# Kernel optimization log

Measured on AMD Instinct MI355X. Metric: run time of the kernel, lower is better.

## Reference

```python
import jax, jax.numpy as jnp
import numpy as np

N_NODES = 20000
N_EDGES = 320000
N_GRAPHS = 64


def gat_conv(x, src, dst, W, a_src, a_dst, bias, heads, ch, concat):
    # x: [N, F_in]; W: [F_in, heads*ch]; a_src/a_dst: [heads, ch]
    N = x.shape[0]
    h = (x @ W).reshape(N, heads, ch)                       # [N, H, C]
    alpha_s = jnp.sum(h * a_src, axis=-1)                   # [N, H]
    alpha_d = jnp.sum(h * a_dst, axis=-1)                   # [N, H]
    e = jax.nn.leaky_relu(alpha_s[src] + alpha_d[dst], 0.2) # [E, H]
    # segment softmax over incoming edges of each destination node
    m = jax.ops.segment_max(e, dst, num_segments=N)         # [N, H]
    ex = jnp.exp(e - m[dst])
    denom = jax.ops.segment_sum(ex, dst, num_segments=N)    # [N, H]
    alpha = ex / (denom[dst] + 1e-16)                       # [E, H]
    msg = h[src] * alpha[:, :, None]                        # [E, H, C]
    out = jax.ops.segment_sum(msg, dst, num_segments=N)     # [N, H, C]
    out = out.reshape(N, heads * ch) if concat else out.mean(axis=1)
    return out + bias, alpha


def setup_inputs() -> dict:
    key = jax.random.key(0)
    ks = jax.random.split(key, 24)
    dim_in, md, dim_out = 8, 64, 128
    hid = md * 4  # 256
    p = lambda k, shape: jax.random.normal(k, shape, dtype=jnp.float32) * 0.1
    inp = {
        "x_ppi": jax.random.normal(ks[0], (N_NODES, dim_in), dtype=jnp.float32),
        "ppi_edge_index": jax.random.randint(ks[1], (2, N_EDGES), 0, N_NODES),
        "ppi_batch": jnp.sort(jax.random.randint(ks[2], (N_NODES,), 0, N_GRAPHS)),
        # GATConv 1: dim_in -> 64, heads=4, concat
        "W1": p(ks[3], (dim_in, 4 * md)), "a_src1": p(ks[4], (4, md)), "a_dst1": p(ks[5], (4, md)), "b_gat1": jnp.zeros((hid,), jnp.float32),
        "lw1": p(ks[6], (dim_in, hid)), "lb1": jnp.zeros((hid,), jnp.float32),
        # GATConv 2: 256 -> 64, heads=4, concat
        "W2": p(ks[7], (hid, 4 * md)), "a_src2": p(ks[8], (4, md)), "a_dst2": p(ks[9], (4, md)), "b_gat2": jnp.zeros((hid,), jnp.float32),
        "lw2": p(ks[10], (hid, hid)), "lb2": jnp.zeros((hid,), jnp.float32),
        # GATConv 3: 256 -> 128, heads=6, concat=False (mean)
        "W3": p(ks[11], (hid, 6 * dim_out)), "a_src3": p(ks[12], (6, dim_out)), "a_dst3": p(ks[13], (6, dim_out)), "b_gat3": jnp.zeros((dim_out,), jnp.float32),
        "lw3": p(ks[14], (hid, dim_out)), "lb3": jnp.zeros((dim_out,), jnp.float32),
        # BatchNorm1d(dim_out), training-mode batch statistics
        "bn_gamma": jnp.ones((dim_out,), jnp.float32), "bn_beta": jnp.zeros((dim_out,), jnp.float32),
    }
    return inp


def reference(x_ppi, ppi_edge_index, ppi_batch,
              W1, a_src1, a_dst1, b_gat1, lw1, lb1,
              W2, a_src2, a_dst2, b_gat2, lw2, lb2,
              W3, a_src3, a_dst3, b_gat3, lw3, lb3,
              bn_gamma, bn_beta):
    src, dst = ppi_edge_index[0], ppi_edge_index[1]
    g1, _ = gat_conv(x_ppi, src, dst, W1, a_src1, a_dst1, b_gat1, heads=4, ch=64, concat=True)
    x = jax.nn.relu(g1 + x_ppi @ lw1 + lb1)
    g2, _ = gat_conv(x, src, dst, W2, a_src2, a_dst2, b_gat2, heads=4, ch=64, concat=True)
    x = jax.nn.relu(g2 + x @ lw2 + lb2)
    x_res = x @ lw3 + lb3
    g3, att = gat_conv(x, src, dst, W3, a_src3, a_dst3, b_gat3, heads=6, ch=128, concat=False)
    x = g3 + x_res
    x = jax.nn.relu(x)
    # BatchNorm1d, training mode (biased variance, eps=1e-5)
    mu = x.mean(axis=0)
    var = jnp.mean((x - mu) ** 2, axis=0)
    x = (x - mu) * jax.lax.rsqrt(var + 1e-5) * bn_gamma + bn_beta
    # global max pool over graphs
    pooled = jax.ops.segment_max(x, ppi_batch, num_segments=N_GRAPHS)
    return pooled, att
```

## Files before the change

### kernel.cpp

```cpp
#include <hip/hip_runtime.h>
#include <hip/hip_bf16.h>
#include <math.h>

#define N_NODES 20000
#define N_EDGES 320000
#define N_GRAPHS 64

typedef __bf16 bf16_t;
typedef bf16_t bf16x8 __attribute__((ext_vector_type(8)));
typedef bf16_t bf16x4 __attribute__((ext_vector_type(4)));
typedef bf16_t bf16x2 __attribute__((ext_vector_type(2)));
typedef float f32x4 __attribute__((ext_vector_type(4)));
typedef float f32x2 __attribute__((ext_vector_type(2)));

__global__ void hist_k(const int* __restrict__ dst, int* __restrict__ deg, int E) {
    int e = blockIdx.x * 256 + threadIdx.x;
    if (e < E) atomicAdd(&deg[dst[e]], 1);
}

__global__ __launch_bounds__(1024) void scan_k(const int* __restrict__ deg,
                                               int* __restrict__ offs,
                                               int* __restrict__ cursor, int n) {
    __shared__ int s_ws[16];
    int tid = threadIdx.x;
    int lane = tid & 63, w = tid >> 6;
    int carry = 0;
    for (int base = 0; base < n; base += 1024) {
        int i = base + tid;
        int v = (i < n) ? deg[i] : 0;
        int x = v;
        #pragma unroll
        for (int off = 1; off < 64; off <<= 1) {
            int t = __shfl_up(x, off);
            if (lane >= off) x += t;
        }
        if (lane == 63) s_ws[w] = x;
        __syncthreads();
        if (tid < 16) {
            int y = s_ws[tid];
            #pragma unroll
            for (int off = 1; off < 16; off <<= 1) {
                int t = __shfl_up(y, off);
                if (tid >= off) y += t;
            }
            s_ws[tid] = y;
        }
        __syncthreads();
        int wbase = (w > 0) ? s_ws[w - 1] : 0;
        int ex = carry + wbase + x - v;
        if (i < n) { offs[i] = ex; cursor[i] = ex; }
        carry += s_ws[15];
        __syncthreads();
    }
    if (tid == 0) offs[n] = carry;
}

__global__ void scatter_k(const int* __restrict__ src, const int* __restrict__ dst,
                          int* __restrict__ cursor, int* __restrict__ csr_src,
                          int* __restrict__ csr_eid, int E) {
    int e = blockIdx.x * 256 + threadIdx.x;
    if (e < E) {
        int d = dst[e];
        int p = atomicAdd(&cursor[d], 1);
        csr_src[p] = src[e];
        csr_eid[p] = e;
    }
}

__global__ __launch_bounds__(256) void wt_k(const float* __restrict__ W,
                                            bf16_t* __restrict__ Bt, int K, int N) {
    __shared__ float t[32][33];
    int k0 = blockIdx.y * 32, n0 = blockIdx.x * 32;
    int tx = threadIdx.x & 31, ty = threadIdx.x >> 5;
    for (int i = ty; i < 32; i += 8) t[i][tx] = W[(size_t)(k0 + i) * N + n0 + tx];
    __syncthreads();
    for (int i = ty; i < 32; i += 8)
        Bt[(size_t)(n0 + i) * K + k0 + tx] = (bf16_t)t[tx][i];
}

__global__ void w3s_k(const float* __restrict__ W3, const float* __restrict__ lw3,
                      bf16_t* __restrict__ Bt) {
    int id = blockIdx.x * 256 + threadIdx.x;
    if (id >= 128 * 1792) return;
    int n = id / 1792, k = id - n * 1792;
    float v;
    if (k < 1536) {
        int h = k >> 8, c = k & 255;
        v = W3[(size_t)c * 768 + h * 128 + n] * (1.f / 6.f);
    } else {
        int c = k - 1536;
        v = lw3[(size_t)c * 128 + n];
    }
    Bt[id] = (bf16_t)v;
}

__global__ void b40_k(const float* __restrict__ W1, const float* __restrict__ lw1,
                      float* __restrict__ B) {
    int id = blockIdx.x * 256 + threadIdx.x;
    if (id >= 40 * 256) return;
    int k = id >> 8, n = id & 255;
    float v;
    if (k < 32) {
        int h = k >> 3, c = k & 7;
        v = ((n >> 6) == h) ? W1[(size_t)c * 256 + n] : 0.f;
    } else {
        int c = k - 32;
        v = lw1[(size_t)c * 256 + n];
    }
    B[id] = v;
}

__global__ void va_k(const float* __restrict__ W, const float* __restrict__ a_s,
                     const float* __restrict__ a_d, float* __restrict__ Va,
                     float* __restrict__ Vd, int H, int C) {
    int k = blockIdx.x;
    int lane = threadIdx.x;
    const float* wr = W + (size_t)k * H * C;
    for (int h = 0; h < H; ++h) {
        float sa = 0.f, sd = 0.f;
        for (int c = lane; c < C; c += 64) {
            float wv = wr[h * C + c];
            sa += wv * a_s[h * C + c];
            sd += wv * a_d[h * C + c];
        }
        #pragma unroll
        for (int m = 32; m; m >>= 1) { sa += __shfl_xor(sa, m); sd += __shfl_xor(sd, m); }
        if (lane == 0) { Va[k * H + h] = sa; Vd[k * H + h] = sd; }
    }
}

__global__ void addb_k(const float* __restrict__ a, const float* __restrict__ b,
                       float* __restrict__ o, int n) {
    int i = blockIdx.x * 256 + threadIdx.x;
    if (i < n) o[i] = a[i] + b[i];
}

template <typename OUT>
__global__ __launch_bounds__(256) void gemm_k(const float* __restrict__ A,
                                              const float* __restrict__ B,
                                              OUT* __restrict__ C,
                                              const float* __restrict__ bias,
                                              int M, int N, int K, int relu) {
    __shared__ float As[16][65];
    __shared__ float Bs[16][64];
    int tid = threadIdx.x;
    int tx = tid & 15, ty = tid >> 4;
    int row0 = blockIdx.y * 64, col0 = blockIdx.x * 64;
    float acc[4][4] = {};
    for (int k0 = 0; k0 < K; k0 += 16) {
        #pragma unroll
        for (int i = 0; i < 4; ++i) {
            int idx = tid + i * 256;
            int m = idx >> 4, kk = idx & 15;
            int gm = row0 + m, gk = k0 + kk;
            As[kk][m] = (gm < M && gk < K) ? A[(size_t)gm * K + gk] : 0.f;
        }
        #pragma unroll
        for (int i = 0; i < 4; ++i) {
            int idx = tid + i * 256;
            int kk = idx >> 6, n = idx & 63;
            int gk = k0 + kk, gn = col0 + n;
            Bs[kk][n] = (gk < K && gn < N) ? B[(size_t)gk * N + gn] : 0.f;
        }
        __syncthreads();
        #pragma unroll
        for (int kk = 0; kk < 16; ++kk) {
            float a[4], b[4];
            #pragma unroll
            for (int i = 0; i < 4; ++i) a[i] = As[kk][ty * 4 + i];
            #pragma unroll
            for (int j = 0; j < 4; ++j) b[j] = Bs[kk][tx * 4 + j];
            #pragma unroll
            for (int i = 0; i < 4; ++i)
                #pragma unroll
                for (int j = 0; j < 4; ++j) acc[i][j] += a[i] * b[j];
        }
        __syncthreads();
    }
    #pragma unroll
    for (int i = 0; i < 4; ++i) {
        int gm = row0 + ty * 4 + i;
        if (gm >= M) continue;
        #pragma unroll
        for (int j = 0; j < 4; ++j) {
            int gn = col0 + tx * 4 + j;
            if (gn < N) {
                float r = acc[i][j] + (bias ? bias[gn] : 0.f);
                if (relu) r = fmaxf(r, 0.f);
                C[(size_t)gm * N + gn] = (OUT)r;
            }
        }
    }
}

template <typename OUT>
__global__ __launch_bounds__(256) void gemm_bf16_k(
    const bf16_t* __restrict__ A, const bf16_t* __restrict__ Bt,
    OUT* __restrict__ C, const float* __restrict__ bias, int M, int N, int K,
    const float* __restrict__ asv, const float* __restrict__ adv,
    float* __restrict__ as_o, float* __restrict__ ad_o, int H, int Ch, int relu) {
    __shared__ bf16_t As[128][40];
    __shared__ bf16_t Bs[128][40];
    int tid = threadIdx.x;
    int row0 = blockIdx.y * 128, col0 = blockIdx.x * 128;
    int wave = tid >> 6, lane = tid & 63, quad = lane >> 4, l16 = lane & 15;
    int wm = wave >> 1, wn = wave & 1;
    f32x4 acc[4][4] = {};
    int sr = tid >> 2;
    int sc = (tid & 3) * 8;
    for (int k0 = 0; k0 < K; k0 += 32) {
        #pragma unroll
        for (int half = 0; half < 2; ++half) {
            int r = sr + half * 64;
            int gm = row0 + r;
            bf16x8 v = {};
            if (gm < M) v = *(const bf16x8*)&A[(size_t)gm * K + k0 + sc];
            *(bf16x8*)&As[r][sc] = v;
            int gn = col0 + r;
            bf16x8 w = {};
            if (gn < N) w = *(const bf16x8*)&Bt[(size_t)gn * K + k0 + sc];
            *(bf16x8*)&Bs[r][sc] = w;
        }
        __syncthreads();
        bf16x8 af[4], bfr[4];
        #pragma unroll
        for (int i = 0; i < 4; ++i) {
            af[i] = *(const bf16x8*)&As[wm * 64 + i * 16 + l16][quad * 8];
            bfr[i] = *(const bf16x8*)&Bs[wn * 64 + i * 16 + l16][quad * 8];
        }
        #pragma unroll
        for (int i = 0; i < 4; ++i)
            #pragma unroll
            for (int j = 0; j < 4; ++j)
                acc[i][j] = __builtin_amdgcn_mfma_f32_16x16x32_bf16(af[i], bfr[j],
                                                                   acc[i][j], 0, 0, 0);
        __syncthreads();
    }
    #pragma unroll
    for (int i = 0; i < 4; ++i) {
        int base_m = row0 + wm * 64 + i * 16 + quad * 4;
        #pragma unroll
        for (int j = 0; j < 4; ++j) {
            int gn = col0 + wn * 64 + j * 16 + l16;
            float bv = bias ? bias[gn] : 0.f;
            #pragma unroll
            for (int r = 0; r < 4; ++r) {
                int gm = base_m + r;
                if (gm < M) {
                    float rr = acc[i][j][r] + bv;
                    if (relu) rr = fmaxf(rr, 0.f);
                    C[(size_t)gm * N + gn] = (OUT)rr;
                }
            }
        }
    }
    if (asv) {
        int hd = (col0 + wn * 64) / Ch;
        float av[4], dv[4];
        #pragma unroll
        for (int j = 0; j < 4; ++j) {
            int ca = col0 + wn * 64 + j * 16 + l16;
            av[j] = asv[ca];
            dv[j] = adv[ca];
        }
        #pragma unroll
        for (int i = 0; i < 4; ++i) {
            float sp[4] = {}, sd[4] = {};
            #pragma unroll
            for (int j = 0; j < 4; ++j)
                #pragma unroll
                for (int r = 0; r < 4; ++r) {
                    sp[r] += acc[i][j][r] * av[j];
                    sd[r] += acc[i][j][r] * dv[j];
                }
            #pragma unroll
            for (int m = 1; m < 16; m <<= 1)
                #pragma unroll
                for (int r = 0; r < 4; ++r) {
                    sp[r] += __shfl_xor(sp[r], m);
                    sd[r] += __shfl_xor(sd[r], m);
                }
            if (l16 == 0) {
                #pragma unroll
                for (int r = 0; r < 4; ++r) {
                    int gm = row0 + wm * 64 + i * 16 + quad * 4 + r;
                    if (gm < M) {
                        as_o[gm * H + hd] = sp[r];
                        ad_o[gm * H + hd] = sd[r];
                    }
                }
            }
        }
    }
}

__global__ __launch_bounds__(256) void gemm_bf16_thin_k(
    const bf16_t* __restrict__ A, const bf16_t* __restrict__ Bt,
    float* __restrict__ C, const float* __restrict__ bias, int M, int N, int K) {
    __shared__ bf16_t As[32][40];
    __shared__ bf16_t Bs[64][40];
    int tid = threadIdx.x;
    int row0 = blockIdx.y * 32, col0 = blockIdx.x * 64;
    int wave = tid >> 6, lane = tid & 63, quad = lane >> 4, l16 = lane & 15;
    int wr = wave & 1;
    int wc = wave >> 1;
    f32x4 acc[2] = {};
    int ar = tid >> 2, ac = (tid & 3) * 8;
    for (int k0 = 0; k0 < K; k0 += 32) {
        if (tid < 128) {
            int gm = row0 + ar;
            bf16x8 v = {};
            if (gm < M) v = *(const bf16x8*)&A[(size_t)gm * K + k0 + ac];
            *(bf16x8*)&As[ar][ac] = v;
        }
        *(bf16x8*)&Bs[ar][ac] = *(const bf16x8*)&Bt[(size_t)(col0 + ar) * K + k0 + ac];
        __syncthreads();
        bf16x8 af = *(const bf16x8*)&As[wr * 16 + l16][quad * 8];
        #pragma unroll
        for (int j = 0; j < 2; ++j) {
            bf16x8 bf = *(const bf16x8*)&Bs[wc * 32 + j * 16 + l16][quad * 8];
            acc[j] = __builtin_amdgcn_mfma_f32_16x16x32_bf16(af, bf, acc[j], 0, 0, 0);
        }
        __syncthreads();
    }
    #pragma unroll
    for (int j = 0; j < 2; ++j) {
        int gn = col0 + wc * 32 + j * 16 + l16;
        float bv = bias[gn];
        #pragma unroll
        for (int r = 0; r < 4; ++r) {
            int gm = row0 + wr * 16 + quad * 4 + r;
            if (gm < M) C[(size_t)gm * N + gn] = fmaxf(acc[j][r] + bv, 0.f);
        }
    }
}

__device__ __forceinline__ float leaky02(float v) { return v > 0.f ? v : 0.2f * v; }

__global__ void asad1_k(const float* __restrict__ x, const float* __restrict__ Va,
                        const float* __restrict__ Vd, float* __restrict__ as_,
                        float* __restrict__ ad_, int N) {
    int idx = blockIdx.x * 256 + threadIdx.x;
    if (idx >= N * 4) return;
    int j = idx >> 2, h = idx & 3;
    const float* xr = x + (size_t)j * 8;
    float sa = 0.f, sd = 0.f;
    #pragma unroll
    for (int c = 0; c < 8; ++c) {
        sa += xr[c] * Va[c * 4 + h];
        sd += xr[c] * Vd[c * 4 + h];
    }
    as_[idx] = sa;
    ad_[idx] = sd;
}

__global__ void asad3_k(const bf16_t* __restrict__ xb, const float* __restrict__ Va,
                        const float* __restrict__ Vd, float* __restrict__ as_,
                        float* __restrict__ ad_) {
    int j = blockIdx.x;
    int lane = threadIdx.x;
    bf16x4 v = *(const bf16x4*)&xb[(size_t)j * 256 + lane * 4];
    float sa[6] = {}, sd[6] = {};
    #pragma unroll
    for (int i = 0; i < 4; ++i) {
        int k = lane * 4 + i;
        float xv = (float)v[i];
        #pragma unroll
        for (int h = 0; h < 6; ++h) {
            sa[h] += xv * Va[k * 6 + h];
            sd[h] += xv * Vd[k * 6 + h];
        }
    }
    #pragma unroll
    for (int h = 0; h < 6; ++h) {
        float a = sa[h], d = sd[h];
        #pragma unroll
        for (int m = 32; m; m >>= 1) { a += __shfl_xor(a, m); d += __shfl_xor(d, m); }
        if (lane == 0) { as_[j * 6 + h] = a; ad_[j * 6 + h] = d; }
    }
}

__global__ __launch_bounds__(256) void agg_z1_k(
    const float* __restrict__ x, const float* __restrict__ as_,
    const float* __restrict__ ad_, const int* __restrict__ offs,
    const int* __restrict__ csr_src, float* __restrict__ z1) {
    int j = blockIdx.x * 4 + (threadIdx.x >> 6);
    int t = threadIdx.x & 63;
    int e_l = t >> 3, c = t & 7;
    int o0 = offs[j], deg = offs[j + 1] - o0;
    float adj0 = ad_[j * 4 + 0], adj1 = ad_[j * 4 + 1];
    float adj2 = ad_[j * 4 + 2], adj3 = ad_[j * 4 + 3];
    float acc[4] = {}, ws[4] = {};
    for (int e0 = 0; e0 < deg; e0 += 8) {
        int ne = min(8, deg - e0);
        if (e_l < ne) {
            int s = csr_src[o0 + e0 + e_l];
            float xv = x[(size_t)s * 8 + c];
            f32x4 a = *(const f32x4*)&as_[s * 4];
            float w0 = __expf(leaky02(a[0] + adj0));
            float w1 = __expf(leaky02(a[1] + adj1));
            float w2 = __expf(leaky02(a[2] + adj2));
            float w3 = __expf(leaky02(a[3] + adj3));
            acc[0] += w0 * xv; acc[1] += w1 * xv;
            acc[2] += w2 * xv; acc[3] += w3 * xv;
            ws[0] += w0; ws[1] += w1; ws[2] += w2; ws[3] += w3;
        }
    }
    #pragma unroll
    for (int m = 8; m < 64; m <<= 1)
        #pragma unroll
        for (int h = 0; h < 4; ++h) {
            acc[h] += __shfl_xor(acc[h], m);
            ws[h] += __shfl_xor(ws[h], m);
        }
    if (e_l == 0) {
        #pragma unroll
        for (int h = 0; h < 4; ++h)
            z1[(size_t)j * 40 + h * 8 + c] = acc[h] / (ws[h] + 1e-16f);
        z1[(size_t)j * 40 + 32 + c] = x[(size_t)j * 8 + c];
    }
}

__global__ __launch_bounds__(256) void agg_concat_k(
    const bf16_t* __restrict__ h, const float* __restrict__ as_,
    const float* __restrict__ ad_, const int* __restrict__ offs,
    const int* __restrict__ csr_src, const float* __restrict__ lin,
    const float* __restrict__ bgat, bf16_t* __restrict__ xb) {
    int j = blockIdx.x;
    int tid = threadIdx.x;
    int o0 = offs[j], deg = offs[j + 1] - o0;
    __shared__ int s_src[64];
    __shared__ float s_adj[4];
    __shared__ float s_ws[8][4];
    __shared__ float s_inv[4];
    __shared__ float s_red[8][256];
    if (tid < 4) s_adj[tid] = ad_[j * 4 + tid];
    int g = tid >> 5;
    int u = tid & 31;
    int myh = u >> 3;
    const char* hbase = (const char*)h + u * 16;
    f32x4 acc0 = {}, acc1 = {};
    float wsum = 0.f;
    for (int e0 = 0; e0 < deg; e0 += 64) {
        int ne = min(64, deg - e0);
        if (tid < ne) s_src[tid] = csr_src[o0 + e0 + tid];
        __syncthreads();
        float adj = s_adj[myh];
        #pragma unroll 2
        for (int e = g; e < ne; e += 8) {
            int s = s_src[e];
            float w = __expf(leaky02(as_[s * 4 + myh] + adj));
            bf16x8 v = *(const bf16x8*)(hbase + (size_t)s * 512);
            wsum += w;
            #pragma unroll
            for (int i = 0; i < 4; ++i) acc0[i] += w * (float)v[i];
            #pragma unroll
            for (int i = 0; i < 4; ++i) acc1[i] += w * (float)v[4 + i];
        }
        __syncthreads();
    }
    if ((u & 7) == 0) s_ws[g][myh] = wsum;
    *(f32x4*)&s_red[g][u * 8] = acc0;
    *(f32x4*)&s_red[g][u * 8 + 4] = acc1;
    __syncthreads();
    if (tid < 4) {
        float d = 0.f;
        #pragma unroll
        for (int g2 = 0; g2 < 8; ++g2) d += s_ws[g2][tid];
        s_inv[tid] = 1.f / (d + 1e-16f);
    }
    __syncthreads();
    {
        int c = tid;
        float s = 0.f;
        #pragma unroll
        for (int g2 = 0; g2 < 8; ++g2) s += s_red[g2][c];
        float v = fmaxf(s * s_inv[c >> 6] + bgat[c] + lin[(size_t)j * 256 + c], 0.f);
        xb[(size_t)j * 256 + c] = (bf16_t)v;
    }
}

__global__ __launch_bounds__(192) void agg_z3_k(
    const bf16_t* __restrict__ xb, const float* __restrict__ as_,
    const float* __restrict__ ad_, const int* __restrict__ offs,
    const int* __restrict__ csr_src, const int* __restrict__ csr_eid,
    bf16_t* __restrict__ z, float* __restrict__ att) {
    int j = blockIdx.x;
    int tid = threadIdx.x;
    int o0 = offs[j], deg = offs[j + 1] - o0;
    __shared__ float s_adj[6];
    __shared__ int s_src[64];
    __shared__ float s_w[64 * 6];
    __shared__ float s_inv[6];
    if (tid < 6) s_adj[tid] = ad_[j * 6 + tid];
    __syncthreads();
    int h = tid >> 5;
    int c = tid & 31;
    const char* xbase = (const char*)xb + c * 16;
    f32x4 a0 = {}, a1 = {};
    float wsum = 0.f;
    for (int e0 = 0; e0 < deg; e0 += 64) {
        int ne = min(64, deg - e0);
        #pragma unroll
        for (int base = 0; base < 2; ++base) {
            int idx = tid + base * 192;
            if (idx < ne * 6) {
                int e = idx / 6, hh = idx - e * 6;
                int s = csr_src[o0 + e0 + e];
                if (hh == 0) s_src[e] = s;
                s_w[idx] = __expf(leaky02(as_[s * 6 + hh] + s_adj[hh]));
            }
        }
        __syncthreads();
        #pragma unroll 4
        for (int e = 0; e < ne; ++e) {
            int s = s_src[e];
            float w = s_w[e * 6 + h];
            bf16x8 v = *(const bf16x8*)(xbase + (size_t)s * 512);
            wsum += w;
            #pragma unroll
            for (int i = 0; i < 4; ++i) a0[i] += w * (float)v[i];
            #pragma unroll
            for (int i = 0; i < 4; ++i) a1[i] += w * (float)v[4 + i];
        }
        __syncthreads();
    }
    float inv = 1.f / (wsum + 1e-16f);
    {
        bf16x8 o;
        #pragma unroll
        for (int i = 0; i < 4; ++i) o[i] = (bf16_t)(a0[i] * inv);
        #pragma unroll
        for (int i = 0; i < 4; ++i) o[4 + i] = (bf16_t)(a1[i] * inv);
        *(bf16x8*)&z[(size_t)j * 1792 + h * 256 + c * 8] = o;
    }
    if (tid < 32)
        *(bf16x8*)&z[(size_t)j * 1792 + 1536 + tid * 8] =
            *(const bf16x8*)&xb[(size_t)j * 256 + tid * 8];
    if (c == 0) s_inv[h] = inv;
    __syncthreads();
    for (int idx = tid; idx < deg * 6; idx += 192) {
        int e = idx / 6, hh = idx - e * 6;
        int p = o0 + e;
        int s = csr_src[p];
        att[(size_t)csr_eid[p] * 6 + hh] =
            __expf(leaky02(as_[s * 6 + hh] + s_adj[hh])) * s_inv[hh];
    }
}

__global__ void bn_stats_k(const float* __restrict__ y, float* __restrict__ sums, int N) {
    int c = threadIdx.x;
    float s = 0.f, q = 0.f;
    for (int r = blockIdx.x; r < N; r += gridDim.x) {
        float v = y[(size_t)r * 128 + c];
        s += v;
        q += v * v;
    }
    atomicAdd(&sums[c], s);
    atomicAdd(&sums[128 + c], q);
}
__global__ void bn_scale_k(const float* __restrict__ sums, const float* __restrict__ gamma,
                           const float* __restrict__ beta, float* __restrict__ scale,
                           float* __restrict__ shift, int N) {
    int c = threadIdx.x;
    float mu = sums[c] / (float)N;
    float var = fmaxf(sums[128 + c] / (float)N - mu * mu, 0.f);
    float inv = rsqrtf(var + 1e-5f) * gamma[c];
    scale[c] = inv;
    shift[c] = beta[c] - mu * inv;
}

__device__ __forceinline__ unsigned f2key(float f) {
    unsigned b = __float_as_uint(f);
    return (b & 0x80000000u) ? ~b : (b | 0x80000000u);
}
__global__ void pool_init_k(unsigned* __restrict__ pool_u) {
    int i = blockIdx.x * 256 + threadIdx.x;
    if (i < N_GRAPHS * 128) pool_u[i] = f2key(-3.402823466e38f * 2.0f);
}
__global__ void norm_pool_k(const float* __restrict__ y, const float* __restrict__ scale,
                            const float* __restrict__ shift, const int* __restrict__ batch,
                            unsigned* __restrict__ pool_u, int N) {
    int idx = blockIdx.x * 256 + threadIdx.x;
    if (idx >= N * 128) return;
    int n = idx >> 7, c = idx & 127;
    float v = y[idx] * scale[c] + shift[c];
    atomicMax(&pool_u[batch[n] * 128 + c], f2key(v));
}
__global__ void pool_write_k(const unsigned* __restrict__ pool_u, float* __restrict__ out) {
    int i = blockIdx.x * 256 + threadIdx.x;
    if (i < N_GRAPHS * 128) {
        unsigned u = pool_u[i];
        unsigned b = (u & 0x80000000u) ? (u & 0x7FFFFFFFu) : ~u;
        out[i] = __uint_as_float(b);
    }
}

extern "C" void kernel_launch(void* const* d_in, const int* in_sizes, int n_in,
                              void* d_out, int out_size, void* d_ws, size_t ws_size,
                              hipStream_t stream) {
    const int N = N_NODES, E = N_EDGES;
    const float* x_ppi = (const float*)d_in[0];
    const int* edge = (const int*)d_in[1];
    const int* batch = (const int*)d_in[2];
    const float* W1 = (const float*)d_in[3];
    const float* a_src1 = (const float*)d_in[4];
    const float* a_dst1 = (const float*)d_in[5];
    const float* b_gat1 = (const float*)d_in[6];
    const float* lw1 = (const float*)d_in[7];
    const float* lb1 = (const float*)d_in[8];
    const float* W2 = (const float*)d_in[9];
    const float* a_src2 = (const float*)d_in[10];
    const float* a_dst2 = (const float*)d_in[11];
    const float* b_gat2 = (const float*)d_in[12];
    const float* lw2 = (const float*)d_in[13];
    const float* lb2 = (const float*)d_in[14];
    const float* W3 = (const float*)d_in[15];
    const float* a_src3 = (const float*)d_in[16];
    const float* a_dst3 = (const float*)d_in[17];
    const float* b_gat3 = (const float*)d_in[18];
    const float* lw3 = (const float*)d_in[19];
    const float* lb3 = (const float*)d_in[20];
    const float* bn_gamma = (const float*)d_in[21];
    const float* bn_beta = (const float*)d_in[22];

    const int* src = edge;
    const int* dst = edge + E;

    size_t off = 0;
    auto alloc = [&](size_t bytes) {
        size_t o = off;
        off = (off + bytes + 255) & ~(size_t)255;
        return o;
    };
    char* ws = (char*)d_ws;
    bf16_t* xb = (bf16_t*)(ws + alloc((size_t)N * 256 * 2));
    bf16_t* zbig = (bf16_t*)(ws + alloc((size_t)N * 1792 * 2));
    bf16_t* hb = zbig;
    bf16_t* z3 = zbig;
    float* lin = (float*)(ws + alloc((size_t)N * 256 * 4));
    float* z1 = (float*)(ws + alloc((size_t)N * 40 * 4));
    float* as_ = (float*)(ws + alloc((size_t)N * 6 * 4));
    float* ad_ = (float*)(ws + alloc((size_t)N * 6 * 4));
    int* deg = (int*)(ws + alloc((size_t)(N + 1) * 4));
    int* offs = (int*)(ws + alloc((size_t)(N + 1) * 4));
    int* cursor = (int*)(ws + alloc((size_t)(N + 1) * 4));
    int* csr_src = (int*)(ws + alloc((size_t)E * 4));
    int* csr_eid = (int*)(ws + alloc((size_t)E * 4));
    bf16_t* Wt2 = (bf16_t*)(ws + alloc((size_t)256 * 256 * 2));
    bf16_t* lwt2 = (bf16_t*)(ws + alloc((size_t)256 * 256 * 2));
    bf16_t* Bt3s = (bf16_t*)(ws + alloc((size_t)128 * 1792 * 2));
    float* B40 = (float*)(ws + alloc((size_t)40 * 256 * 4));
    float* Va1 = (float*)(ws + alloc(8 * 4 * 4));
    float* Vd1 = (float*)(ws + alloc(8 * 4 * 4));
    float* Va3 = (float*)(ws + alloc(256 * 6 * 4));
    float* Vd3 = (float*)(ws + alloc(256 * 6 * 4));
    float* bias1s = (float*)(ws + alloc(256 * 4));
    float* bias3s = (float*)(ws + alloc(128 * 4));
    float* bn_sums = (float*)(ws + alloc(256 * 4));
    float* bn_scale = (float*)(ws + alloc(128 * 4));
    float* bn_shift = (float*)(ws + alloc(128 * 4));
    unsigned* pool_u = (unsigned*)(ws + alloc((size_t)N_GRAPHS * 128 * 4));

    float* out_pool = (float*)d_out;
    float* out_att = (float*)d_out + N_GRAPHS * 128;

    hipMemsetAsync(deg, 0, (size_t)N * 4, stream);
    hist_k<<<(E + 255) / 256, 256, 0, stream>>>(dst, deg, E);
    scan_k<<<1, 1024, 0, stream>>>(deg, offs, cursor, N);
    scatter_k<<<(E + 255) / 256, 256, 0, stream>>>(src, dst, cursor, csr_src, csr_eid, E);
    wt_k<<<dim3(8, 8), 256, 0, stream>>>(W2, Wt2, 256, 256);
    wt_k<<<dim3(8, 8), 256, 0, stream>>>(lw2, lwt2, 256, 256);
    w3s_k<<<896, 256, 0, stream>>>(W3, lw3, Bt3s);
    b40_k<<<40, 256, 0, stream>>>(W1, lw1, B40);
    va_k<<<8, 64, 0, stream>>>(W1, a_src1, a_dst1, Va1, Vd1, 4, 64);
    va_k<<<256, 64, 0, stream>>>(W3, a_src3, a_dst3, Va3, Vd3, 6, 128);
    addb_k<<<1, 256, 0, stream>>>(lb1, b_gat1, bias1s, 256);
    addb_k<<<1, 128, 0, stream>>>(lb3, b_gat3, bias3s, 128);

    asad1_k<<<(N * 4 + 255) / 256, 256, 0, stream>>>(x_ppi, Va1, Vd1, as_, ad_, N);
    agg_z1_k<<<N / 4, 256, 0, stream>>>(x_ppi, as_, ad_, offs, csr_src, z1);
    gemm_k<bf16_t><<<dim3(4, 313), 256, 0, stream>>>(z1, B40, xb, bias1s, N, 256, 40, 1);

    gemm_bf16_k<bf16_t><<<dim3(2, 157), 256, 0, stream>>>(xb, Wt2, hb, nullptr, N, 256, 256,
                                                          a_src2, a_dst2, as_, ad_, 4, 64, 0);
    gemm_bf16_k<float><<<dim3(2, 157), 256, 0, stream>>>(xb, lwt2, lin, lb2, N, 256, 256,
                                                         nullptr, nullptr, nullptr, nullptr,
                                                         0, 1, 0);
    agg_concat_k<<<N, 256, 0, stream>>>(hb, as_, ad_, offs, csr_src, lin, b_gat2, xb);

    float* y = lin;
    asad3_k<<<N, 64, 0, stream>>>(xb, Va3, Vd3, as_, ad_);
    agg_z3_k<<<N, 192, 0, stream>>>(xb, as_, ad_, offs, csr_src, csr_eid, z3, out_att);
    gemm_bf16_thin_k<<<dim3(2, 625), 256, 0, stream>>>(z3, Bt3s, y, bias3s, N, 128, 1792);

    hipMemsetAsync(bn_sums, 0, 256 * 4, stream);
    bn_stats_k<<<160, 128, 0, stream>>>(y, bn_sums, N);
    bn_scale_k<<<1, 128, 0, stream>>>(bn_sums, bn_gamma, bn_beta, bn_scale, bn_shift, N);

    pool_init_k<<<(N_GRAPHS * 128 + 255) / 256, 256, 0, stream>>>(pool_u);
    norm_pool_k<<<((size_t)N * 128 + 255) / 256, 256, 0, stream>>>(y, bn_scale, bn_shift, batch,
                                                                   pool_u, N);
    pool_write_k<<<(N_GRAPHS * 128 + 255) / 256, 256, 0, stream>>>(pool_u, out_pool);
}
```

Before: 466.1 us.

## Compute layer-3 per-head weighted aggregation with MFMA over edge tiles

Rewrites agg_z3_k so that, for each chunk of 32 incoming edges, it stages the bf16 attention weights (6 heads padded to 16) and the gathered neighbour features (transposed) in shared memory. It then computes the weighted sums for all heads at once with 16x16x32 bf16 MFMA, replacing the scalar per-head FMA loop. Neighbour rows are now gathered once per chunk and shared by all heads instead of being reloaded by every head group. The trade-offs are rounding the weights to bf16, wasted MFMA rows from the head padding, a transpose through LDS with possible bank conflicts, and a block size raised from 192 to 256.

Result: slower. 503.1 us (+7.9%).

```diff
diff --git a/kernel.cpp b/kernel.cpp
--- a/kernel.cpp
+++ b/kernel.cpp
@@ -480,7 +480,7 @@
     }
 }
 
-__global__ __launch_bounds__(192) void agg_z3_k(
+__global__ __launch_bounds__(256) void agg_z3_k(
     const bf16_t* __restrict__ xb, const float* __restrict__ as_,
     const float* __restrict__ ad_, const int* __restrict__ offs,
     const int* __restrict__ csr_src, const int* __restrict__ csr_eid,
@@ -489,57 +489,79 @@
     int tid = threadIdx.x;
     int o0 = offs[j], deg = offs[j + 1] - o0;
     __shared__ float s_adj[6];
-    __shared__ int s_src[64];
-    __shared__ float s_w[64 * 6];
+    __shared__ int s_src[32];
+    __shared__ bf16_t s_wb[16][32];
+    __shared__ bf16_t s_XT[256][34];
+    __shared__ float s_wp[192];
     __shared__ float s_inv[6];
     if (tid < 6) s_adj[tid] = ad_[j * 6 + tid];
+    int wave = tid >> 6, lane = tid & 63, quad = lane >> 4, l16 = lane & 15;
+    int we = tid / 6, wh = tid - we * 6;
+    int se = tid >> 3, scp = tid & 7;
+    f32x4 acc[4] = {};
+    float wrun = 0.f;
     __syncthreads();
-    int h = tid >> 5;
-    int c = tid & 31;
-    const char* xbase = (const char*)xb + c * 16;
-    f32x4 a0 = {}, a1 = {};
-    float wsum = 0.f;
-    for (int e0 = 0; e0 < deg; e0 += 64) {
-        int ne = min(64, deg - e0);
-        #pragma unroll
-        for (int base = 0; base < 2; ++base) {
-            int idx = tid + base * 192;
-            if (idx < ne * 6) {
-                int e = idx / 6, hh = idx - e * 6;
-                int s = csr_src[o0 + e0 + e];
-                if (hh == 0) s_src[e] = s;
-                s_w[idx] = __expf(leaky02(as_[s * 6 + hh] + s_adj[hh]));
+    for (int e0 = 0; e0 < deg; e0 += 32) {
+        int ne = min(32, deg - e0);
+        if (tid < 32) s_src[tid] = (tid < ne) ? csr_src[o0 + e0 + tid] : -1;
+        if (tid >= 64 && tid < 128) {
+            f32x4 zz = {};
+            *(f32x4*)((char*)s_wb + (tid - 64) * 16) = zz;
+        }
+        __syncthreads();
+        if (tid < 192 && we < ne) {
+            int s = s_src[we];
+            float w = __expf(leaky02(as_[s * 6 + wh] + s_adj[wh]));
+            wrun += w;
+            s_wb[wh][we] = (bf16_t)w;
+        }
+        {
+            int s2 = s_src[se];
+            #pragma unroll
+            for (int i = 0; i < 4; ++i) {
+                int ch0 = (scp * 4 + i) * 8;
+                bf16x8 v = {};
+                if (s2 >= 0) v = *(const bf16x8*)&xb[(size_t)s2 * 256 + ch0];
+                #pragma unroll
+                for (int q = 0; q < 8; ++q) s_XT[ch0 + q][se] = v[q];
             }
         }
         __syncthreads();
-        #pragma unroll 4
-        for (int e = 0; e < ne; ++e) {
-            int s = s_src[e];
-            float w = s_w[e * 6 + h];
-            bf16x8 v = *(const bf16x8*)(xbase + (size_t)s * 512);
-            wsum += w;
-            #pragma unroll
-            for (int i = 0; i < 4; ++i) a0[i] += w * (float)v[i];
-            #pragma unroll
-            for (int i = 0; i < 4; ++i) a1[i] += w * (float)v[4 + i];
-        }
-        __syncthreads();
-    }
-    float inv = 1.f / (wsum + 1e-16f);
-    {
-        bf16x8 o;
-        #pragma unroll
-        for (int i = 0; i < 4; ++i) o[i] = (bf16_t)(a0[i] * inv);
-        #pragma unroll
-        for (int i = 0; i < 4; ++i) o[4 + i] = (bf16_t)(a1[i] * inv);
-        *(bf16x8*)&z[(size_t)j * 1792 + h * 256 + c * 8] = o;
+        bf16x8 af = *(const bf16x8*)&s_wb[l16][quad * 8];
+        #pragma unroll
+        for (int tn = 0; tn < 4; ++tn) {
+            int n0 = (wave * 4 + tn) * 16;
+            bf16x8 bf = *(const bf16x8*)&s_XT[n0 + l16][quad * 8];
+            acc[tn] = __builtin_amdgcn_mfma_f32_16x16x32_bf16(af, bf, acc[tn], 0, 0, 0);
+        }
+        __syncthreads();
+    }
+    if (tid < 192) s_wp[tid] = wrun;
+    __syncthreads();
+    if (tid < 6) {
+        float d = 0.f;
+        #pragma unroll
+        for (int k = 0; k < 32; ++k) d += s_wp[k * 6 + tid];
+        s_inv[tid] = 1.f / (d + 1e-16f);
+    }
+    __syncthreads();
+    if (quad < 2) {
+        #pragma unroll
+        for (int tn = 0; tn < 4; ++tn) {
+            int n0 = (wave * 4 + tn) * 16;
+            #pragma unroll
+            for (int r = 0; r < 4; ++r) {
+                int h = quad * 4 + r;
+                if (h < 6)
+                    z[(size_t)j * 1792 + h * 256 + n0 + l16] =
+                        (bf16_t)(acc[tn][r] * s_inv[h]);
+            }
+        }
     }
     if (tid < 32)
         *(bf16x8*)&z[(size_t)j * 1792 + 1536 + tid * 8] =
             *(const bf16x8*)&xb[(size_t)j * 256 + tid * 8];
-    if (c == 0) s_inv[h] = inv;
-    __syncthreads();
-    for (int idx = tid; idx < deg * 6; idx += 192) {
+    for (int idx = tid; idx < deg * 6; idx += 256) {
         int e = idx / 6, hh = idx - e * 6;
         int p = o0 + e;
         int s = csr_src[p];
@@ -691,7 +713,7 @@
 
     float* y = lin;
     asad3_k<<<N, 64, 0, stream>>>(xb, Va3, Vd3, as_, ad_);
-    agg_z3_k<<<N, 192, 0, stream>>>(xb, as_, ad_, offs, csr_src, csr_eid, z3, out_att);
+    agg_z3_k<<<N, 256, 0, stream>>>(xb, as_, ad_, offs, csr_src, csr_eid, z3, out_att);
     gemm_bf16_thin_k<<<dim3(2, 625), 256, 0, stream>>>(z3, Bt3s, y, bias3s, N, 128, 1792);
 
     hipMemsetAsync(bn_sums, 0, 256 * 4, stream);
```
